# Performance work log

Measured on AMD Instinct MI355X. Metric: run time of the kernel, lower is better.

Reference implementation:

```python
import jax, jax.numpy as jnp
import numpy as np

B, N, L, D, H = 8, 128, 4096, 1024, 16

def setup_inputs() -> dict:
    key = jax.random.key(0)
    ks = jax.random.split(key, 7)
    s = 1.0 / np.sqrt(D)  # xavier-ish scale for square D x D weights
    return {
        "q": jax.random.normal(ks[0], (B, N, D), dtype=jnp.float32),
        "k": jax.random.normal(ks[1], (B, L, D), dtype=jnp.float32),
        "v": jax.random.normal(ks[2], (B, L, D), dtype=jnp.float32),
        "Wq": jax.random.normal(ks[3], (D, D), dtype=jnp.float32) * s,
        "Wk": jax.random.normal(ks[4], (D, D), dtype=jnp.float32) * s,
        "Wv": jax.random.normal(ks[5], (D, D), dtype=jnp.float32) * s,
        "Wo": jax.random.normal(ks[6], (D, D), dtype=jnp.float32) * s,
    }

def reference(q, k, v, Wq, Wk, Wv, Wo):
    Bq, Nq, Dm = q.shape
    Lk = k.shape[1]
    Hh = H
    Dh = Dm // Hh
    scale = Dm ** (-0.5)  # note: scaled by d_model, not head_dim (faithful to source)
    # projections (nn.Linear with weight (out,in): y = x @ W.T)
    qh = (q @ Wq.T).reshape(Bq, Nq, Hh, Dh).transpose(0, 2, 1, 3)  # B H N Dh
    kh = (k @ Wk.T).reshape(Bq, Lk, Hh, Dh).transpose(0, 2, 1, 3)  # B H L Dh
    vh = (v @ Wv.T).reshape(Bq, Lk, Hh, Dh).transpose(0, 2, 1, 3)  # B H L Dh
    attn = jnp.einsum('bhnc,bhlc->bhnl', qh * scale, kh)          # B H N L
    # inverted attention: softmax over the query (N) axis...
    attn = jax.nn.softmax(attn, axis=2)
    # ...then L1-renormalize over the key (L) axis
    attn = attn / jnp.sum(attn, axis=-1, keepdims=True)
    out = jnp.einsum('bhnl,bhlc->bhnc', attn, vh)                 # B H N Dh
    out = out.transpose(0, 2, 1, 3).reshape(Bq, Nq, Dm)
    return out @ Wo.T
```

## Files before the change

### kernel.cpp

```cpp
#include <hip/hip_runtime.h>
#include <stdint.h>

typedef __bf16 bf16_t;
typedef __bf16 bf16x4 __attribute__((ext_vector_type(4)));
typedef __bf16 bf16x8 __attribute__((ext_vector_type(8)));
typedef float f32x4 __attribute__((ext_vector_type(4)));
typedef unsigned int u32;

constexpr int CB = 8, CN = 128, CL = 4096, CD = 1024, CH = 16, CDh = 64;

#define BAR()                                    \
  do {                                           \
    __asm__ volatile("" ::: "memory");           \
    __builtin_amdgcn_s_barrier();                \
    __asm__ volatile("" ::: "memory");           \
  } while (0)

__device__ __forceinline__ bf16x4 cvt4(float4 v) {
  bf16x4 r;
  r[0] = (__bf16)v.x; r[1] = (__bf16)v.y; r[2] = (__bf16)v.z; r[3] = (__bf16)v.w;
  return r;
}

__device__ __forceinline__ void async16(void* lds, const void* g) {
  __builtin_amdgcn_global_load_lds(
      (const __attribute__((address_space(1))) u32*)g,
      (__attribute__((address_space(3))) u32*)lds, 16, 0, 0);
}

__global__ __launch_bounds__(256) void cvt_f32_bf16(const float* __restrict__ in,
                                                    bf16_t* __restrict__ outp, int n4) {
  int i = (int)blockIdx.x * 256 + (int)threadIdx.x;
  if (i < n4) {
    float4 v = reinterpret_cast<const float4*>(in)[i];
    reinterpret_cast<bf16x4*>(outp)[i] = cvt4(v);
  }
}

__global__ __launch_bounds__(512, 2)
void gemm8(const bf16_t* __restrict__ A, const bf16_t* __restrict__ Bw,
           bf16_t* __restrict__ C, int mblocks, int N, int K) {
  __shared__ __attribute__((aligned(16))) char lds[131072];

  const int t = (int)threadIdx.x;
  const int lane = t & 63, w = t >> 6;
  const int wave_m = w >> 2, wave_n = w & 3;
  const int fr = lane & 15, fq = lane >> 4;
  const int bid = (int)blockIdx.x;
  const int x = bid & 7, j = bid >> 3;
  const int S = mblocks >> 3;
  const int nnb = N >> 8;
  const int mb = x * S + (j / nnb);
  const int nb = j % nnb;
  const int brow = mb * 256, bcol = nb * 256;

  auto Aoff = [](int buf, int half) { return (buf * 2 + half) * 16384; };
  auto Boff = [](int buf, int half) { return 65536 + (buf * 2 + half) * 16384; };

  auto stage = [&](int tile, bool dA, bool dB) {
    const int buf = tile & 1;
    const int k0 = tile << 6;
#pragma unroll
    for (int n = 0; n < 2; ++n) {
      const int idx = n * 512 + t;
      const int row = idx >> 3;
      const int u = (idx & 7) ^ (row & 7);
      const int dst = (n * 8 + w) * 1024;
      if (dB) {
#pragma unroll
        for (int h = 0; h < 2; ++h)
          async16(lds + Boff(buf, h) + dst,
                  Bw + (size_t)(bcol + h * 128 + row) * K + k0 + u * 8);
      }
      if (dA) {
#pragma unroll
        for (int h = 0; h < 2; ++h)
          async16(lds + Aoff(buf, h) + dst,
                  A + (size_t)(brow + h * 128 + row) * K + k0 + u * 8);
      }
    }
  };

  bf16x8 af[4][2], blo[2][2], bhi[2][2];
  auto rdA = [&](int buf, int mq) {
    const char* base = lds + Aoff(buf, wave_m);
#pragma unroll
    for (int mf = 0; mf < 4; ++mf) {
      const int row = mq * 64 + mf * 16 + fr;
#pragma unroll
      for (int ks = 0; ks < 2; ++ks)
        af[mf][ks] = *(const bf16x8*)(base + row * 128 + (((ks * 4 + fq) ^ (row & 7)) << 4));
    }
  };
  auto rdB = [&](bf16x8 (&bf)[2][2], int buf, int nq) {
    const char* base = lds + Boff(buf, wave_n >> 1);
#pragma unroll
    for (int nf = 0; nf < 2; ++nf) {
      const int row = (wave_n & 1) * 64 + (nq * 2 + nf) * 16 + fr;
#pragma unroll
      for (int ks = 0; ks < 2; ++ks)
        bf[nf][ks] = *(const bf16x8*)(base + row * 128 + (((ks * 4 + fq) ^ (row & 7)) << 4));
    }
  };

  const f32x4 z = {0.f, 0.f, 0.f, 0.f};
  f32x4 acc[8][4];
#pragma unroll
  for (int m = 0; m < 8; ++m)
#pragma unroll
    for (int n = 0; n < 4; ++n) acc[m][n] = z;

  auto mma = [&](const bf16x8 (&bf)[2][2], int mq, int nq) {
    __builtin_amdgcn_s_setprio(1);
#pragma unroll
    for (int mf = 0; mf < 4; ++mf)
#pragma unroll
      for (int nf = 0; nf < 2; ++nf)
#pragma unroll
        for (int ks = 0; ks < 2; ++ks)
          acc[mq * 4 + mf][nq * 2 + nf] = __builtin_amdgcn_mfma_f32_16x16x32_bf16(
              af[mf][ks], bf[nf][ks], acc[mq * 4 + mf][nq * 2 + nf], 0, 0, 0);
    __builtin_amdgcn_s_setprio(0);
  };

  const int nt = K >> 6;
  stage(0, true, true);
  stage(1, true, true);
  asm volatile("s_waitcnt vmcnt(8)" ::: "memory");
  BAR();

  for (int i = 0; i < nt; ++i) {
    const int buf = i & 1;
    rdA(buf, 0);
    rdB(blo, buf, 0);
    BAR();
    mma(blo, 0, 0);
    BAR();
    rdB(bhi, buf, 1);
    BAR();
    mma(bhi, 0, 1);
    BAR();
    rdA(buf, 1);
    if (i + 2 < nt) stage(i + 2, false, true);
    BAR();
    mma(blo, 1, 0);
    BAR();
    if (i + 2 < nt) stage(i + 2, true, false);
    if (i == nt - 2) {
      asm volatile("s_waitcnt vmcnt(0)" ::: "memory");
    } else if (i < nt - 2) {
      asm volatile("s_waitcnt vmcnt(8)" ::: "memory");
    }
    BAR();
    mma(bhi, 1, 1);
    BAR();
  }

#pragma unroll
  for (int mf = 0; mf < 8; ++mf)
#pragma unroll
    for (int nf = 0; nf < 4; ++nf)
#pragma unroll
      for (int r = 0; r < 4; ++r) {
        const int row = brow + wave_m * 128 + mf * 16 + fq * 4 + r;
        const int col = bcol + wave_n * 64 + nf * 16 + fr;
        C[(size_t)row * N + col] = (__bf16)acc[mf][nf][r];
      }
}

template<bool CF32>
__global__ __launch_bounds__(256)
void gemm_dma(const bf16_t* __restrict__ Ab, const bf16_t* __restrict__ Bw,
              void* __restrict__ Cp, int mblocks, int N, int K) {
  __shared__ __attribute__((aligned(16))) char AsB[2][8192];
  __shared__ __attribute__((aligned(16))) char BsB[2][8192];

  const int t = (int)threadIdx.x;
  const int lane = t & 63, wv = t >> 6;
  const int bid = (int)blockIdx.x;
  const int x = bid & 7;
  const int j = bid >> 3;
  const int S = mblocks >> 3;
  const int mb = (S > 0) ? (x * S + (j >> 3)) : (j >> 3);
  const int nb = j & 7;
  const int brow = mb * 128;
  const int bcol = nb * 128;
  const int wm = (wv >> 1) * 64, wn = (wv & 1) * 64;
  const int fr = lane & 15, fq = lane >> 4;

  auto stageT = [&](char* dst, const bf16_t* src, int rbase, int k0) {
    const int r4 = lane >> 2, u = lane & 3;
#pragma unroll
    for (int i = 0; i < 2; ++i) {
      const int seg = i * 4 + wv;
      const int row = seg * 16 + r4;
      const int col = ((u ^ ((row >> 1) & 3)) << 3);
      async16(dst + seg * 1024, src + (size_t)(rbase + row) * K + k0 + col);
    }
  };

  const f32x4 z = {0.f, 0.f, 0.f, 0.f};
  f32x4 acc[4][4];
#pragma unroll
  for (int m = 0; m < 4; ++m)
#pragma unroll
    for (int n = 0; n < 4; ++n) acc[m][n] = z;

  const int nt = K >> 5;
  stageT(AsB[0], Ab, brow, 0);
  stageT(BsB[0], Bw, bcol, 0);
  __syncthreads();
  int cur = 0;

  for (int tt = 0; tt < nt; ++tt) {
    if (tt + 1 < nt) {
      stageT(AsB[cur ^ 1], Ab, brow, (tt + 1) << 5);
      stageT(BsB[cur ^ 1], Bw, bcol, (tt + 1) << 5);
    }
    const char* Ac = AsB[cur];
    const char* Bc = BsB[cur];

    bf16x8 af[4], bfg[4];
#pragma unroll
    for (int m = 0; m < 4; ++m) {
      const int R = wm + m * 16 + fr;
      const int ph = (fq << 4) ^ (((R >> 1) & 3) << 4);
      af[m] = *(const bf16x8*)(Ac + R * 64 + ph);
    }
#pragma unroll
    for (int n = 0; n < 4; ++n) {
      const int R = wn + n * 16 + fr;
      const int ph = (fq << 4) ^ (((R >> 1) & 3) << 4);
      bfg[n] = *(const bf16x8*)(Bc + R * 64 + ph);
    }
#pragma unroll
    for (int m = 0; m < 4; ++m)
#pragma unroll
      for (int n = 0; n < 4; ++n)
        acc[m][n] = __builtin_amdgcn_mfma_f32_16x16x32_bf16(af[m], bfg[n], acc[m][n], 0, 0, 0);

    __syncthreads();
    cur ^= 1;
  }

  const int rb = fq * 4;
#pragma unroll
  for (int m = 0; m < 4; ++m)
#pragma unroll
    for (int n = 0; n < 4; ++n)
#pragma unroll
      for (int r = 0; r < 4; ++r) {
        const int row = brow + wm + m * 16 + rb + r;
        const int col = bcol + wn + n * 16 + fr;
        if constexpr (CF32)
          ((float*)Cp)[(size_t)row * N + col] = acc[m][n][r];
        else
          ((bf16_t*)Cp)[(size_t)row * N + col] = (__bf16)acc[m][n][r];
      }
}

template<bool A_IS_F32, bool C_IS_F32>
__global__ __launch_bounds__(256)
void gemm_bt(const void* __restrict__ Ap, const float* __restrict__ Bw,
             void* __restrict__ Cp, int M, int N, int K) {
  (void)M;
  __shared__ bf16_t As[128][40];
  __shared__ bf16_t Bs[128][40];
  const int t = (int)threadIdx.x;
  const int lane = t & 63, wv = t >> 6;
  const int wm = (wv >> 1) * 64, wn = (wv & 1) * 64;
  const int brow = (int)blockIdx.y * 128, bcol = (int)blockIdx.x * 128;
  const int fr = lane & 15, fk = (lane >> 4) * 8;

  const f32x4 z = {0.f, 0.f, 0.f, 0.f};
  f32x4 acc[4][4];
#pragma unroll
  for (int m = 0; m < 4; ++m)
#pragma unroll
    for (int n = 0; n < 4; ++n) acc[m][n] = z;

  for (int k0 = 0; k0 < K; k0 += 32) {
    if constexpr (A_IS_F32) {
      const float* A = (const float*)Ap;
      const int tr = t >> 3, tc = (t & 7) * 4;
#pragma unroll
      for (int p = 0; p < 4; ++p) {
        const int r = p * 32 + tr;
        float4 v = *reinterpret_cast<const float4*>(A + (size_t)(brow + r) * K + k0 + tc);
        *reinterpret_cast<bf16x4*>(&As[r][tc]) = cvt4(v);
      }
    } else {
      const bf16_t* A = (const bf16_t*)Ap;
      const int tr = t >> 2, tc = (t & 3) * 8;
#pragma unroll
      for (int p = 0; p < 2; ++p) {
        const int r = p * 64 + tr;
        *reinterpret_cast<int4*>(&As[r][tc]) =
            *reinterpret_cast<const int4*>(A + (size_t)(brow + r) * K + k0 + tc);
      }
    }
    {
      const int tr = t >> 3, tc = (t & 7) * 4;
#pragma unroll
      for (int p = 0; p < 4; ++p) {
        const int r = p * 32 + tr;
        float4 v = *reinterpret_cast<const float4*>(Bw + (size_t)(bcol + r) * K + k0 + tc);
        *reinterpret_cast<bf16x4*>(&Bs[r][tc]) = cvt4(v);
      }
    }
    __syncthreads();
    bf16x8 af[4], bfr[4];
#pragma unroll
    for (int m = 0; m < 4; ++m)
      af[m] = *reinterpret_cast<const bf16x8*>(&As[wm + m * 16 + fr][fk]);
#pragma unroll
    for (int n = 0; n < 4; ++n)
      bfr[n] = *reinterpret_cast<const bf16x8*>(&Bs[wn + n * 16 + fr][fk]);
#pragma unroll
    for (int m = 0; m < 4; ++m)
#pragma unroll
      for (int n = 0; n < 4; ++n)
        acc[m][n] = __builtin_amdgcn_mfma_f32_16x16x32_bf16(af[m], bfr[n], acc[m][n], 0, 0, 0);
    __syncthreads();
  }
  const int rb = (lane >> 4) * 4;
#pragma unroll
  for (int m = 0; m < 4; ++m)
#pragma unroll
    for (int n = 0; n < 4; ++n)
#pragma unroll
      for (int r = 0; r < 4; ++r) {
        const int row = brow + wm + m * 16 + rb + r;
        const int col = bcol + wn + n * 16 + fr;
        if constexpr (C_IS_F32)
          ((float*)Cp)[(size_t)row * N + col] = acc[m][n][r];
        else
          ((bf16_t*)Cp)[(size_t)row * N + col] = (__bf16)acc[m][n][r];
      }
}

template<bool DIRECT>
__global__ __launch_bounds__(256)
void attn_inv(const bf16_t* __restrict__ qh, const bf16_t* __restrict__ kh,
              const bf16_t* __restrict__ vh, bf16_t* __restrict__ ao,
              float* __restrict__ part, int lcount) {
  const int bh = (int)blockIdx.x;
  const int b = bh >> 4, h = bh & 15;
  const int l_begin = (int)blockIdx.y * lcount;

  __shared__ bf16_t Qs[128][72];
  __shared__ bf16_t Ks[64][72];
  __shared__ bf16_t Vt[80][72];
  __shared__ bf16_t Ps[128][72];

  const int t = (int)threadIdx.x;
  const int lane = t & 63, w = t >> 6;
  const int fr = lane & 15, fq = lane >> 4;

  const bf16_t* qb = qh + (size_t)(b * CN) * CD + h * CDh;
#pragma unroll
  for (int p = 0; p < 4; ++p) {
    const int j = p * 256 + t;
    const int r = j >> 3, cc = (j & 7) * 8;
    *reinterpret_cast<int4*>(&Qs[r][cc]) =
        *reinterpret_cast<const int4*>(qb + (size_t)r * CD + cc);
  }
#pragma unroll
  for (int p = 0; p < 4; ++p) {
    const int j = p * 256 + t;
    const int r = 64 + (j >> 6), c = j & 63;
    Vt[r][c] = (r == 64) ? (__bf16)1.0f : (__bf16)0.0f;
  }

  const f32x4 z = {0.f, 0.f, 0.f, 0.f};
  f32x4 acc[2][5];
#pragma unroll
  for (int m = 0; m < 2; ++m)
#pragma unroll
    for (int n = 0; n < 5; ++n) acc[m][n] = z;

  for (int l0 = l_begin; l0 < l_begin + lcount; l0 += 64) {
    __syncthreads();
    const bf16_t* kb = kh + (size_t)(b * CL + l0) * CD + h * CDh;
    const bf16_t* vb = vh + (size_t)(b * CL + l0) * CD + h * CDh;
#pragma unroll
    for (int p = 0; p < 2; ++p) {
      const int j = p * 256 + t;
      const int r = j >> 3, cc = (j & 7) * 8;
      *reinterpret_cast<int4*>(&Ks[r][cc]) =
          *reinterpret_cast<const int4*>(kb + (size_t)r * CD + cc);
      int4 vv = *reinterpret_cast<const int4*>(vb + (size_t)r * CD + cc);
      const bf16_t* hp = reinterpret_cast<const bf16_t*>(&vv);
#pragma unroll
      for (int i = 0; i < 8; ++i) Vt[cc + i][r] = hp[i];
    }
    __syncthreads();

    f32x4 s[8];
#pragma unroll
    for (int m = 0; m < 8; ++m) s[m] = z;
#pragma unroll
    for (int ks = 0; ks < 2; ++ks) {
      bf16x8 bk = *reinterpret_cast<const bf16x8*>(&Ks[w * 16 + fr][ks * 32 + fq * 8]);
#pragma unroll
      for (int m = 0; m < 8; ++m) {
        bf16x8 aq = *reinterpret_cast<const bf16x8*>(&Qs[m * 16 + fr][ks * 32 + fq * 8]);
        s[m] = __builtin_amdgcn_mfma_f32_16x16x32_bf16(aq, bk, s[m], 0, 0, 0);
      }
    }

    float p[8][4];
    float mx = -3.0e38f;
#pragma unroll
    for (int m = 0; m < 8; ++m)
#pragma unroll
      for (int r = 0; r < 4; ++r) {
        const float xv = s[m][r] * 0.03125f;
        p[m][r] = xv;
        mx = fmaxf(mx, xv);
      }
    mx = fmaxf(mx, __shfl_xor(mx, 16));
    mx = fmaxf(mx, __shfl_xor(mx, 32));
    float sum = 0.f;
#pragma unroll
    for (int m = 0; m < 8; ++m)
#pragma unroll
      for (int r = 0; r < 4; ++r) {
        const float e = __expf(p[m][r] - mx);
        p[m][r] = e;
        sum += e;
      }
    sum += __shfl_xor(sum, 16);
    sum += __shfl_xor(sum, 32);
    const float inv = 1.0f / sum;
    const int pcol = w * 16 + fr;
#pragma unroll
    for (int m = 0; m < 8; ++m)
#pragma unroll
      for (int r = 0; r < 4; ++r)
        Ps[m * 16 + fq * 4 + r][pcol] = (__bf16)(p[m][r] * inv);
    __syncthreads();

#pragma unroll
    for (int ks = 0; ks < 2; ++ks) {
      bf16x8 pa[2];
#pragma unroll
      for (int m = 0; m < 2; ++m)
        pa[m] = *reinterpret_cast<const bf16x8*>(&Ps[w * 32 + m * 16 + fr][ks * 32 + fq * 8]);
#pragma unroll
      for (int n = 0; n < 5; ++n) {
        bf16x8 bv = *reinterpret_cast<const bf16x8*>(&Vt[n * 16 + fr][ks * 32 + fq * 8]);
#pragma unroll
        for (int m = 0; m < 2; ++m)
          acc[m][n] = __builtin_amdgcn_mfma_f32_16x16x32_bf16(pa[m], bv, acc[m][n], 0, 0, 0);
      }
    }
  }

  if constexpr (DIRECT) {
    bf16_t* ob = ao + (size_t)(b * CN) * CD + h * CDh;
#pragma unroll
    for (int m = 0; m < 2; ++m)
#pragma unroll
      for (int r = 0; r < 4; ++r) {
        const float R = __shfl(acc[m][4][r], lane & 48);
        const float invr = 1.0f / R;
        const int row = w * 32 + m * 16 + fq * 4 + r;
#pragma unroll
        for (int n = 0; n < 4; ++n) {
          const int col = n * 16 + fr;
          ob[(size_t)row * CD + col] = (__bf16)(acc[m][n][r] * invr);
        }
      }
  } else {
    float* pb = part + ((size_t)blockIdx.y * (CB * CH) + bh) * (size_t)(CN * 72);
#pragma unroll
    for (int m = 0; m < 2; ++m)
#pragma unroll
      for (int r = 0; r < 4; ++r) {
        const int row = w * 32 + m * 16 + fq * 4 + r;
#pragma unroll
        for (int n = 0; n < 4; ++n)
          pb[(size_t)row * 72 + n * 16 + fr] = acc[m][n][r];
        if (fr == 0) pb[(size_t)row * 72 + 64] = acc[m][4][r];
      }
  }
}

__global__ __launch_bounds__(256)
void attn_reduce(const float* __restrict__ part, bf16_t* __restrict__ ao, int nsplit) {
  const int idx = (int)blockIdx.x * 256 + (int)threadIdx.x;
  const int c = idx & 63;
  const int n = (idx >> 6) & 127;
  const int bh = idx >> 13;
  const float* p = part + (size_t)bh * (CN * 72) + (size_t)n * 72;
  const size_t sstr = (size_t)(CB * CH) * (CN * 72);
  float o = 0.f, r = 0.f;
  for (int s = 0; s < nsplit; ++s) {
    o += p[(size_t)s * sstr + c];
    r += p[(size_t)s * sstr + 64];
  }
  const int b = bh >> 4, h = bh & 15;
  ao[((size_t)(b * CN + n)) * CD + h * CDh + c] = (__bf16)(o / r);
}

extern "C" void kernel_launch(void* const* d_in, const int* in_sizes, int n_in,
                              void* d_out, int out_size, void* d_ws, size_t ws_size,
                              hipStream_t stream) {
  (void)in_sizes; (void)n_in; (void)out_size;
  const float* q  = (const float*)d_in[0];
  const float* k  = (const float*)d_in[1];
  const float* v  = (const float*)d_in[2];
  const float* Wq = (const float*)d_in[3];
  const float* Wk = (const float*)d_in[4];
  const float* Wv = (const float*)d_in[5];
  const float* Wo = (const float*)d_in[6];
  float* out = (float*)d_out;

  const size_t MiB = (size_t)1 << 20;
  const size_t QH_OFF = 0;
  const size_t KH_OFF = 2 * MiB;
  const size_t VH_OFF = KH_OFF + 64 * MiB;
  const size_t AO_OFF = VH_OFF + 64 * MiB;
  const size_t FIXED  = AO_OFF + 2 * MiB;
  if (ws_size < FIXED) return;

  char* ws = (char*)d_ws;
  bf16_t* qh = (bf16_t*)(ws + QH_OFF);
  bf16_t* kh = (bf16_t*)(ws + KH_OFF);
  bf16_t* vh = (bf16_t*)(ws + VH_OFF);
  bf16_t* ao = (bf16_t*)(ws + AO_OFF);

  const int M_q = CB * CN;
  const int M_kv = CB * CL;
  const int W4 = CD * CD / 4;
  const int A4_kv = M_kv * CD / 4;
  const int A4_q  = M_q * CD / 4;

  const size_t WBUF_OFF = FIXED;
  const size_t QC_OFF   = WBUF_OFF + 2 * MiB;
  const size_t KC_OFF   = QC_OFF + 2 * MiB;
  const size_t NEED_FAST = KC_OFF + 64 * MiB;

  if (ws_size >= NEED_FAST) {
    bf16_t* wbuf = (bf16_t*)(ws + WBUF_OFF);
    bf16_t* qc   = (bf16_t*)(ws + QC_OFF);
    bf16_t* kc   = (bf16_t*)(ws + KC_OFF);
    float*  part = (float*)(ws + KC_OFF);

    cvt_f32_bf16<<<A4_q / 256, 256, 0, stream>>>(q, qc, A4_q);
    cvt_f32_bf16<<<W4 / 256, 256, 0, stream>>>(Wq, wbuf, W4);
    gemm_dma<false><<<(M_q / 128) * 8, 256, 0, stream>>>(qc, wbuf, qh, M_q / 128, CD, CD);

    cvt_f32_bf16<<<A4_kv / 256, 256, 0, stream>>>(k, kc, A4_kv);
    cvt_f32_bf16<<<W4 / 256, 256, 0, stream>>>(Wk, wbuf, W4);
    gemm8<<<(M_kv / 256) * (CD / 256), 512, 0, stream>>>(kc, wbuf, kh, M_kv / 256, CD, CD);

    cvt_f32_bf16<<<A4_kv / 256, 256, 0, stream>>>(v, kc, A4_kv);
    cvt_f32_bf16<<<W4 / 256, 256, 0, stream>>>(Wv, wbuf, W4);
    gemm8<<<(M_kv / 256) * (CD / 256), 512, 0, stream>>>(kc, wbuf, vh, M_kv / 256, CD, CD);

    attn_inv<false><<<dim3(CB * CH, 8), 256, 0, stream>>>(qh, kh, vh, ao, part, CL / 8);
    attn_reduce<<<(CB * CH * CN * 64) / 256, 256, 0, stream>>>(part, ao, 8);

    cvt_f32_bf16<<<W4 / 256, 256, 0, stream>>>(Wo, wbuf, W4);
    gemm_dma<true><<<(M_q / 128) * 8, 256, 0, stream>>>(ao, wbuf, out, M_q / 128, CD, CD);
    return;
  }

  gemm_bt<true, false><<<dim3(CD / 128, M_q / 128),  256, 0, stream>>>(q, Wq, qh, M_q,  CD, CD);
  gemm_bt<true, false><<<dim3(CD / 128, M_kv / 128), 256, 0, stream>>>(k, Wk, kh, M_kv, CD, CD);
  gemm_bt<true, false><<<dim3(CD / 128, M_kv / 128), 256, 0, stream>>>(v, Wv, vh, M_kv, CD, CD);
  attn_inv<true><<<dim3(CB * CH, 1), 256, 0, stream>>>(qh, kh, vh, ao, nullptr, CL);
  gemm_bt<false, true><<<dim3(CD / 128, M_q / 128), 256, 0, stream>>>(ao, Wo, out, M_q, CD, CD);
}
```

Before: 340.2 us.

## Fuse fp32-to-bf16 conversion of K/V activations into the projection GEMM A-load

The K and V projection GEMM now reads fp32 activations directly, converting them to bf16 in registers and writing swizzled tiles to LDS. This removes the standalone conversion passes over the 128 MiB k and v inputs and their bf16 round trip through memory. The four weight conversions are batched into one launch. The cost is register-staged A loads in place of async DMA, plus extra waitcnt and LDS writes inside the main loop, which may reduce overlap or occupancy.

Result: slower. 375.4 us (+10.3%).

```diff
diff --git a/kernel.cpp b/kernel.cpp
--- a/kernel.cpp
+++ b/kernel.cpp
@@ -21,6 +21,12 @@
   r[0] = (__bf16)v.x; r[1] = (__bf16)v.y; r[2] = (__bf16)v.z; r[3] = (__bf16)v.w;
   return r;
 }
+__device__ __forceinline__ bf16x8 cvt8f(const float4& a, const float4& b) {
+  bf16x8 r;
+  r[0] = (__bf16)a.x; r[1] = (__bf16)a.y; r[2] = (__bf16)a.z; r[3] = (__bf16)a.w;
+  r[4] = (__bf16)b.x; r[5] = (__bf16)b.y; r[6] = (__bf16)b.z; r[7] = (__bf16)b.w;
+  return r;
+}
 
 __device__ __forceinline__ void async16(void* lds, const void* g) {
   __builtin_amdgcn_global_load_lds(
@@ -37,9 +43,21 @@
   }
 }
 
+__global__ __launch_bounds__(256)
+void cvt_w4(const float* __restrict__ Wq, const float* __restrict__ Wk,
+            const float* __restrict__ Wv, const float* __restrict__ Wo,
+            bf16_t* __restrict__ outp, int n4) {
+  const float* srcs[4] = {Wq, Wk, Wv, Wo};
+  const float* s = srcs[blockIdx.y];
+  int i = (int)blockIdx.x * 256 + (int)threadIdx.x;
+  if (i < n4)
+    reinterpret_cast<bf16x4*>(outp + (size_t)blockIdx.y * CD * CD)[i] =
+        cvt4(reinterpret_cast<const float4*>(s)[i]);
+}
+
 __global__ __launch_bounds__(512, 2)
-void gemm8(const bf16_t* __restrict__ A, const bf16_t* __restrict__ Bw,
-           bf16_t* __restrict__ C, int mblocks, int N, int K) {
+void gemm8f(const float* __restrict__ Af, const bf16_t* __restrict__ Bw,
+            bf16_t* __restrict__ C, int mblocks, int N, int K) {
   __shared__ __attribute__((aligned(16))) char lds[131072];
 
   const int t = (int)threadIdx.x;
@@ -57,7 +75,7 @@
   auto Aoff = [](int buf, int half) { return (buf * 2 + half) * 16384; };
   auto Boff = [](int buf, int half) { return 65536 + (buf * 2 + half) * 16384; };
 
-  auto stage = [&](int tile, bool dA, bool dB) {
+  auto stageB = [&](int tile) {
     const int buf = tile & 1;
     const int k0 = tile << 6;
 #pragma unroll
@@ -66,18 +84,31 @@
       const int row = idx >> 3;
       const int u = (idx & 7) ^ (row & 7);
       const int dst = (n * 8 + w) * 1024;
-      if (dB) {
-#pragma unroll
-        for (int h = 0; h < 2; ++h)
-          async16(lds + Boff(buf, h) + dst,
-                  Bw + (size_t)(bcol + h * 128 + row) * K + k0 + u * 8);
-      }
-      if (dA) {
-#pragma unroll
-        for (int h = 0; h < 2; ++h)
-          async16(lds + Aoff(buf, h) + dst,
-                  A + (size_t)(brow + h * 128 + row) * K + k0 + u * 8);
-      }
+#pragma unroll
+      for (int h = 0; h < 2; ++h)
+        async16(lds + Boff(buf, h) + dst,
+                Bw + (size_t)(bcol + h * 128 + row) * K + k0 + u * 8);
+    }
+  };
+
+  float4 ra[8];
+  const int arow = t >> 1, ahf = t & 1;
+  auto loadA = [&](int tile) {
+    const float* src = Af + (size_t)(brow + arow) * K + (tile << 6) + ahf * 32;
+#pragma unroll
+    for (int c = 0; c < 4; ++c) {
+      ra[2 * c]     = *reinterpret_cast<const float4*>(src + c * 8);
+      ra[2 * c + 1] = *reinterpret_cast<const float4*>(src + c * 8 + 4);
+    }
+  };
+  auto writeA = [&](int tile) {
+    const int buf = tile & 1;
+    char* base = lds + Aoff(buf, arow >> 7) + (arow & 127) * 128;
+#pragma unroll
+    for (int c = 0; c < 4; ++c) {
+      const int u = ahf * 4 + c;
+      const int ph = u ^ (arow & 7);
+      *reinterpret_cast<bf16x8*>(base + ph * 16) = cvt8f(ra[2 * c], ra[2 * c + 1]);
     }
   };
 
@@ -124,13 +155,17 @@
   };
 
   const int nt = K >> 6;
-  stage(0, true, true);
-  stage(1, true, true);
+  loadA(0);
+  stageB(0);
+  stageB(1);
   asm volatile("s_waitcnt vmcnt(8)" ::: "memory");
+  writeA(0);
+  asm volatile("s_waitcnt vmcnt(4) lgkmcnt(0)" ::: "memory");
   BAR();
 
   for (int i = 0; i < nt; ++i) {
     const int buf = i & 1;
+    if (i + 1 < nt) loadA(i + 1);
     rdA(buf, 0);
     rdB(blo, buf, 0);
     BAR();
@@ -141,15 +176,18 @@
     mma(bhi, 0, 1);
     BAR();
     rdA(buf, 1);
-    if (i + 2 < nt) stage(i + 2, false, true);
+    if (i + 2 < nt) stageB(i + 2);
     BAR();
     mma(blo, 1, 0);
     BAR();
-    if (i + 2 < nt) stage(i + 2, true, false);
-    if (i == nt - 2) {
-      asm volatile("s_waitcnt vmcnt(0)" ::: "memory");
-    } else if (i < nt - 2) {
-      asm volatile("s_waitcnt vmcnt(8)" ::: "memory");
+    if (i + 1 < nt) {
+      if (i + 2 < nt) {
+        asm volatile("s_waitcnt vmcnt(4)" ::: "memory");
+      } else {
+        asm volatile("s_waitcnt vmcnt(0)" ::: "memory");
+      }
+      writeA(i + 1);
+      asm volatile("s_waitcnt lgkmcnt(0)" ::: "memory");
     }
     BAR();
     mma(bhi, 1, 1);
@@ -534,37 +572,32 @@
   const int M_q = CB * CN;
   const int M_kv = CB * CL;
   const int W4 = CD * CD / 4;
-  const int A4_kv = M_kv * CD / 4;
-  const int A4_q  = M_q * CD / 4;
-
-  const size_t WBUF_OFF = FIXED;
-  const size_t QC_OFF   = WBUF_OFF + 2 * MiB;
-  const size_t KC_OFF   = QC_OFF + 2 * MiB;
-  const size_t NEED_FAST = KC_OFF + 64 * MiB;
+  const int A4_q = M_q * CD / 4;
+
+  const size_t WB4_OFF  = FIXED;
+  const size_t QC_OFF   = WB4_OFF + 8 * MiB;
+  const size_t PART_OFF = QC_OFF + 2 * MiB;
+  const size_t PB = (size_t)CB * CH * CN * 72 * 4;
+  const size_t NEED_FAST = PART_OFF + 8 * PB;
 
   if (ws_size >= NEED_FAST) {
-    bf16_t* wbuf = (bf16_t*)(ws + WBUF_OFF);
-    bf16_t* qc   = (bf16_t*)(ws + QC_OFF);
-    bf16_t* kc   = (bf16_t*)(ws + KC_OFF);
-    float*  part = (float*)(ws + KC_OFF);
+    bf16_t* wb4 = (bf16_t*)(ws + WB4_OFF);
+    bf16_t* qc  = (bf16_t*)(ws + QC_OFF);
+    float* part = (float*)(ws + PART_OFF);
+    const size_t WS = (size_t)CD * CD;
+
+    cvt_w4<<<dim3(W4 / 256, 4), 256, 0, stream>>>(Wq, Wk, Wv, Wo, wb4, W4);
 
     cvt_f32_bf16<<<A4_q / 256, 256, 0, stream>>>(q, qc, A4_q);
-    cvt_f32_bf16<<<W4 / 256, 256, 0, stream>>>(Wq, wbuf, W4);
-    gemm_dma<false><<<(M_q / 128) * 8, 256, 0, stream>>>(qc, wbuf, qh, M_q / 128, CD, CD);
-
-    cvt_f32_bf16<<<A4_kv / 256, 256, 0, stream>>>(k, kc, A4_kv);
-    cvt_f32_bf16<<<W4 / 256, 256, 0, stream>>>(Wk, wbuf, W4);
-    gemm8<<<(M_kv / 256) * (CD / 256), 512, 0, stream>>>(kc, wbuf, kh, M_kv / 256, CD, CD);
-
-    cvt_f32_bf16<<<A4_kv / 256, 256, 0, stream>>>(v, kc, A4_kv);
-    cvt_f32_bf16<<<W4 / 256, 256, 0, stream>>>(Wv, wbuf, W4);
-    gemm8<<<(M_kv / 256) * (CD / 256), 512, 0, stream>>>(kc, wbuf, vh, M_kv / 256, CD, CD);
+    gemm_dma<false><<<(M_q / 128) * 8, 256, 0, stream>>>(qc, wb4, qh, M_q / 128, CD, CD);
+
+    gemm8f<<<(M_kv / 256) * (CD / 256), 512, 0, stream>>>(k, wb4 + WS, kh, M_kv / 256, CD, CD);
+    gemm8f<<<(M_kv / 256) * (CD / 256), 512, 0, stream>>>(v, wb4 + 2 * WS, vh, M_kv / 256, CD, CD);
 
     attn_inv<false><<<dim3(CB * CH, 8), 256, 0, stream>>>(qh, kh, vh, ao, part, CL / 8);
     attn_reduce<<<(CB * CH * CN * 64) / 256, 256, 0, stream>>>(part, ao, 8);
 
-    cvt_f32_bf16<<<W4 / 256, 256, 0, stream>>>(Wo, wbuf, W4);
-    gemm_dma<true><<<(M_q / 128) * 8, 256, 0, stream>>>(ao, wbuf, out, M_q / 128, CD, CD);
+    gemm_dma<true><<<(M_q / 128) * 8, 256, 0, stream>>>(ao, wb4 + 3 * WS, out, M_q / 128, CD, CD);
     return;
   }
 
```
